# Performance work log

Hardware: AMD Instinct MI355X
Metric: run time of the kernel (lower is better)

## Reference

```python
import jax, jax.numpy as jnp
import numpy as np

ALPHA = 0.2  # LeakyReLU negative slope
NEG_INF = -9e15


def setup_inputs() -> dict:
    key = jax.random.key(0)
    k1, k2, k3, k4, k5 = jax.random.split(key, 5)
    B, N, F_in, F_out = 1, 8192, 256, 128
    h = jax.random.normal(k1, (B, N, F_in), dtype=jnp.float32)
    adj_mat = jax.random.randint(k2, (B, N, N), 0, 2, dtype=jnp.int32)
    W = jax.random.normal(k3, (F_out, F_in), dtype=jnp.float32) * 0.05
    b = jax.random.normal(k4, (F_out,), dtype=jnp.float32) * 0.05
    a = jax.random.normal(k5, (2 * F_out, 1), dtype=jnp.float32) * 0.05
    return {"h": h, "adj_mat": adj_mat, "W": W, "b": b, "a": a}


def reference(h, adj_mat, W, b, a):
    # Wh: (B, N, F_out)
    Wh = jnp.einsum('bnf,of->bno', h, W) + b
    F_out = W.shape[0]
    # Original builds concat[Wh_i, Wh_j] @ a. Equivalent: a1.Wh_i + a2.Wh_j.
    a1 = a[:F_out, 0]
    a2 = a[F_out:, 0]
    s1 = Wh @ a1  # (B, N) source-i contribution
    s2 = Wh @ a2  # (B, N) source-j contribution
    e = s1[:, :, None] + s2[:, None, :]  # (B, N, N)
    e = jnp.where(e >= 0, e, ALPHA * e)  # LeakyReLU
    e = jnp.where(adj_mat > 0, e, NEG_INF)
    attention = jax.nn.softmax(e, axis=1)  # softmax over dim=1, as in the source
    h_prime = jnp.einsum('bij,bjf->bif', attention, Wh)
    return jax.nn.elu(h_prime)
```

## Files before the change

### kernel.cpp

```cpp
#include <hip/hip_runtime.h>

#define NN 8192
#define FI 256
#define FO 128
#define GAT_ALPHA 0.2f

typedef _Float16 f16x8 __attribute__((ext_vector_type(8)));
typedef _Float16 f16x2 __attribute__((ext_vector_type(2)));
typedef float f32x4 __attribute__((ext_vector_type(4)));
typedef unsigned char uchar;
typedef unsigned int uint32;

__global__ __launch_bounds__(256) void k1_wh(const float* __restrict__ h,
                                             const float* __restrict__ W,
                                             const float* __restrict__ bias,
                                             float* __restrict__ Wh) {
  __shared__ float hs[32][FI + 1];
  __shared__ float wt[32][FO];
  const int t = threadIdx.x;
  const int j0 = blockIdx.x * 32;
  {
    const int row = t >> 3, c0 = (t & 7) * 32;
    const float* src = h + (size_t)(j0 + row) * FI + c0;
#pragma unroll
    for (int e = 0; e < 8; ++e) {
      float4 v = *(const float4*)(src + 4 * e);
      hs[row][c0 + 4 * e + 0] = v.x;
      hs[row][c0 + 4 * e + 1] = v.y;
      hs[row][c0 + 4 * e + 2] = v.z;
      hs[row][c0 + 4 * e + 3] = v.w;
    }
  }
  const int f4 = (t & 31) * 4;
  const int r0 = (t >> 5) * 4;
  float acc[4][4];
#pragma unroll
  for (int r = 0; r < 4; ++r)
#pragma unroll
    for (int e = 0; e < 4; ++e) acc[r][e] = 0.f;

  for (int kc = 0; kc < FI; kc += 32) {
    __syncthreads();
    {
      const int f = t >> 1, kb = (t & 1) * 16;
      const float* wsrc = W + (size_t)f * FI + kc + kb;
#pragma unroll
      for (int e = 0; e < 16; ++e) wt[kb + e][f] = wsrc[e];
    }
    __syncthreads();
#pragma unroll
    for (int k = 0; k < 32; ++k) {
      const float4 wv = *(const float4*)&wt[k][f4];
      float hv[4];
#pragma unroll
      for (int r = 0; r < 4; ++r) hv[r] = hs[r0 + r][kc + k];
#pragma unroll
      for (int r = 0; r < 4; ++r) {
        acc[r][0] += hv[r] * wv.x;
        acc[r][1] += hv[r] * wv.y;
        acc[r][2] += hv[r] * wv.z;
        acc[r][3] += hv[r] * wv.w;
      }
    }
  }
  const float4 bv = *(const float4*)&bias[f4];
#pragma unroll
  for (int r = 0; r < 4; ++r) {
    float4 o;
    o.x = acc[r][0] + bv.x;
    o.y = acc[r][1] + bv.y;
    o.z = acc[r][2] + bv.z;
    o.w = acc[r][3] + bv.w;
    *(float4*)&Wh[(size_t)(j0 + r0 + r) * FO + f4] = o;
  }
}

__global__ __launch_bounds__(256) void k1b_sv(const float* __restrict__ Wh,
                                              const float* __restrict__ a,
                                              float4* __restrict__ r4,
                                              float4* __restrict__ c4,
                                              float2* __restrict__ r2,
                                              _Float16* __restrict__ ey16,
                                              _Float16* __restrict__ ez16,
                                              float* __restrict__ s2x,
                                              float* __restrict__ corr) {
  if (blockIdx.x == 0 && threadIdx.x < FO) corr[threadIdx.x] = 0.f;
  const int lane = threadIdx.x & 63;
  const int j = blockIdx.x * 4 + (threadIdx.x >> 6);
  const float* row = Wh + (size_t)j * FO;
  const float w0 = row[lane], w1 = row[lane + 64];
  float s1 = w0 * a[lane] + w1 * a[lane + 64];
  float s2 = w0 * a[FO + lane] + w1 * a[FO + lane + 64];
#pragma unroll
  for (int o = 32; o >= 1; o >>= 1) {
    s1 += __shfl_xor(s1, o);
    s2 += __shfl_xor(s2, o);
  }
  if (lane == 0) {
    const float e1 = expf(s1), e1a = expf(GAT_ALPHA * s1);
    const float e2 = expf(s2), e2a = expf(GAT_ALPHA * s2);
    float4 rv; rv.x = s1; rv.y = e1; rv.z = e1a; rv.w = 0.f;
    float4 cv; cv.x = s2; cv.y = e2; cv.z = e2a; cv.w = 0.f;
    r4[j] = rv;
    c4[j] = cv;
    r2[j] = make_float2(e1, e1a);
    ey16[j] = (_Float16)e2;
    ez16[j] = (_Float16)e2a;
    s2x[j] = s2;
  }
}

__global__ __launch_bounds__(256) void k2_stats(const int* __restrict__ adj,
                                                const float4* __restrict__ r4,
                                                const float* __restrict__ s2x,
                                                uchar* __restrict__ bitsB,
                                                float2* __restrict__ zpart) {
  __shared__ float4 rs[64];
  const int t = threadIdx.x;
  const int jc = blockIdx.x & 3;
  const int ic = blockIdx.x >> 2;
  const int i0 = ic * 64;
  const int j0 = jc * 2048 + t * 8;
  if (t < 64) rs[t] = r4[i0 + t];
  const float4 ca = *(const float4*)(s2x + j0);
  const float4 cb = *(const float4*)(s2x + j0 + 4);
  const float cx[8] = {ca.x, ca.y, ca.z, ca.w, cb.x, cb.y, cb.z, cb.w};
  float accP[8], accN[8];
#pragma unroll
  for (int e = 0; e < 8; ++e) { accP[e] = 0.f; accN[e] = 0.f; }
  __syncthreads();
  const int4* ap = (const int4*)(adj + (size_t)i0 * NN + j0);
  uchar* bp = bitsB + (size_t)i0 * (NN / 8) + jc * 256 + t;
  for (int ir = 0; ir < 64; ir += 8) {
    int4 av[8][2];
#pragma unroll
    for (int u = 0; u < 8; ++u) {
      av[u][0] = ap[(size_t)(ir + u) * (NN / 4)];
      av[u][1] = ap[(size_t)(ir + u) * (NN / 4) + 1];
    }
#pragma unroll
    for (int u = 0; u < 8; ++u) {
      const float4 ri = rs[ir + u];
      const int aa[8] = {av[u][0].x, av[u][0].y, av[u][0].z, av[u][0].w,
                         av[u][1].x, av[u][1].y, av[u][1].z, av[u][1].w};
      uint32 byte = 0;
#pragma unroll
      for (int e = 0; e < 8; ++e) {
        const bool act = aa[e] > 0;
        byte |= act ? (1u << e) : 0u;
        const bool pos = (ri.x + cx[e]) >= 0.f;
        accP[e] += (act && pos) ? ri.y : 0.f;
        accN[e] += (act && !pos) ? ri.z : 0.f;
      }
      bp[(size_t)(ir + u) * (NN / 8)] = (uchar)byte;
    }
  }
  float2* zp = zpart + (size_t)ic * NN + j0;
#pragma unroll
  for (int e = 0; e < 8; ++e) zp[e] = make_float2(accP[e], accN[e]);
}

__global__ __launch_bounds__(256) void k3_scale(const float* __restrict__ Wh,
                                                const float4* __restrict__ c4,
                                                const float2* __restrict__ zpart,
                                                _Float16* __restrict__ Wfrag,
                                                float* __restrict__ corr) {
  __shared__ float rz[64];
  __shared__ int emp[64];
  __shared__ float2 psum[256];
  __shared__ __align__(16) _Float16 tile[FO * 64];
  const int t = threadIdx.x;
  const int j0 = blockIdx.x * 64;
  {
    const int jl = t & 63, q = t >> 6;
    float p = 0.f, n = 0.f;
    for (int ic = q * 32; ic < q * 32 + 32; ++ic) {
      const float2 z = zpart[(size_t)ic * NN + j0 + jl];
      p += z.x;
      n += z.y;
    }
    psum[t] = make_float2(p, n);
  }
  __syncthreads();
  if (t < 64) {
    const float p = psum[t].x + psum[64 + t].x + psum[128 + t].x + psum[192 + t].x;
    const float n = psum[t].y + psum[64 + t].y + psum[128 + t].y + psum[192 + t].y;
    const float4 cj = c4[j0 + t];
    const float Z = cj.y * p + cj.z * n;
    rz[t] = (Z > 0.f) ? 1.f / Z : 0.f;
    emp[t] = (Z > 0.f) ? 0 : 1;
  }
  __syncthreads();
  const int f = t & 127, half = t >> 7;
  const unsigned swf = (unsigned)((f & 7) << 4);
  for (int r = half; r < 64; r += 2) {
    const float v = Wh[(size_t)(j0 + r) * FO + f];
    *(_Float16*)((char*)tile + f * 128 + (((unsigned)(r * 2)) ^ swf)) =
        (_Float16)(v * rz[r]);
    if (emp[r]) atomicAdd(&corr[f], v * (1.f / 8192.f));
  }
  __syncthreads();
#pragma unroll
  for (int q = 0; q < 4; ++q) {
    const int G = t + 256 * q;
    const int kcfb = G >> 6, gl = G & 63;
    const int kc = kcfb >> 3, fb = kcfb & 7;
    const int gf = fb * 16 + (gl & 15);
    const int jloc = kc * 32 + (gl >> 4) * 8;
    const f16x8 v = *(const f16x8*)((const char*)tile + gf * 128 +
                                    (((unsigned)(jloc * 2)) ^ ((unsigned)((gf & 7) << 4))));
    ((f16x8*)Wfrag)[(size_t)(((j0 >> 5) + kc) * 8 + fb) * 64 + gl] = v;
  }
}

#define BARRIER_LDS()                                          \
  do {                                                         \
    __builtin_amdgcn_sched_barrier(0);                         \
    asm volatile("s_waitcnt lgkmcnt(0)" ::: "memory");         \
    __builtin_amdgcn_s_barrier();                              \
    __builtin_amdgcn_sched_barrier(0);                         \
  } while (0)

__global__ __launch_bounds__(512, 4) void k4_main(const uchar* __restrict__ bitsB,
                                                  const float2* __restrict__ r2,
                                                  const _Float16* __restrict__ ey16,
                                                  const _Float16* __restrict__ ez16,
                                                  const _Float16* __restrict__ Wfrag,
                                                  float* __restrict__ part) {
  __shared__ __align__(16) _Float16 P[2][64 * 64];
  __shared__ uint32 lut[256][4];
  const int t = threadIdx.x;
  const int rowtile = blockIdx.x >> 2;
  const int kq = blockIdx.x & 3;
  const int rowbase = rowtile * 64;
  const int koff = kq * 2048;

  if (t < 256) {
#pragma unroll
    for (int p = 0; p < 4; ++p) {
      const uint32 lo = ((t >> (2 * p)) & 1) ? 0x0000FFFFu : 0u;
      const uint32 hi = ((t >> (2 * p + 1)) & 1) ? 0xFFFF0000u : 0u;
      lut[t][p] = lo | hi;
    }
  }

  const int pr = t >> 3, jq = t & 7;
  const float2 rr = r2[rowbase + pr];
  const f16x2 rx2 = {(_Float16)rr.x, (_Float16)rr.x};
  const f16x2 ry2 = {(_Float16)rr.y, (_Float16)rr.y};
  const uchar* bp = bitsB + (size_t)(rowbase + pr) * (NN / 8) + (koff >> 3) + jq;
  const _Float16* eyp = ey16 + koff + jq * 8;
  const _Float16* ezp = ez16 + koff + jq * 8;
  char* const pdst0 = (char*)&P[0][0] + pr * 128 + (((unsigned)(jq * 16)) ^ ((unsigned)((pr & 7) << 4)));
  char* const pdst1 = (char*)&P[1][0] + pr * 128 + (((unsigned)(jq * 16)) ^ ((unsigned)((pr & 7) << 4)));

  const int lane = t & 63, wave = t >> 6;
  const int wr = wave >> 2, wc = wave & 3;
  const int kgrp = lane >> 4, l15 = lane & 15;
  const unsigned asw = (unsigned)((l15 & 7) << 4);
  const int ar0 = (wr * 32 + l15) * 128;
  const int ar1 = ar0 + 16 * 128;

  f32x4 acc00 = {0.f, 0.f, 0.f, 0.f}, acc01 = {0.f, 0.f, 0.f, 0.f};
  f32x4 acc10 = {0.f, 0.f, 0.f, 0.f}, acc11 = {0.f, 0.f, 0.f, 0.f};

  uchar mb0, mb1;
  uint4 ey0, ez0, ey1, ez1;
  f16x8 B000, B001, B010, B011, B100, B101, B110, B111;

#define LOADALL(S, MB, EY, EZ, Bq00, Bq01, Bq10, Bq11)                              \
  do {                                                                              \
    MB = bp[(S) * 8];                                                               \
    EY = *(const uint4*)(eyp + (S) * 64);                                           \
    EZ = *(const uint4*)(ezp + (S) * 64);                                           \
    const _Float16* _b = Wfrag + ((size_t)((kq * 64 + (S) * 2) * 8 + wc * 2) * 64 + lane) * 8; \
    Bq00 = *(const f16x8*)(_b);                                                     \
    Bq01 = *(const f16x8*)(_b + 512);                                               \
    Bq10 = *(const f16x8*)(_b + 4096);                                              \
    Bq11 = *(const f16x8*)(_b + 4096 + 512);                                        \
  } while (0)

#define PGEN(DST, MB, EY, EZ)                                                        \
  do {                                                                               \
    const uint4 _m = *(const uint4*)(&lut[MB][0]);                                   \
    const uint32 _eys[4] = {EY.x, EY.y, EY.z, EY.w};                                 \
    const uint32 _ezs[4] = {EZ.x, EZ.y, EZ.z, EZ.w};                                 \
    const uint32 _ms[4] = {_m.x, _m.y, _m.z, _m.w};                                  \
    uint32 _o[4];                                                                    \
    _Pragma("unroll") for (int _p = 0; _p < 4; ++_p) {                               \
      const f16x2 _a = __builtin_bit_cast(f16x2, _eys[_p]) * rx2;                    \
      const f16x2 _b2 = __builtin_bit_cast(f16x2, _ezs[_p]) * ry2;                   \
      const f16x2 _mx = __builtin_elementwise_max(_a, _b2);                          \
      _o[_p] = __builtin_bit_cast(uint32, _mx) & _ms[_p];                            \
    }                                                                                \
    uint4 _st; _st.x = _o[0]; _st.y = _o[1]; _st.z = _o[2]; _st.w = _o[3];           \
    *(uint4*)(DST) = _st;                                                            \
  } while (0)

#define DO_MFMA(BUF, Bq00, Bq01, Bq10, Bq11)                                        \
  do {                                                                              \
    const char* _Pb = (const char*)&P[BUF][0];                                      \
    const f16x8 a00 = *(const f16x8*)(_Pb + ar0 + ((((unsigned)(kgrp * 16))) ^ asw));        \
    const f16x8 a01 = *(const f16x8*)(_Pb + ar0 + (((unsigned)(64 + kgrp * 16)) ^ asw));     \
    const f16x8 a10 = *(const f16x8*)(_Pb + ar1 + ((((unsigned)(kgrp * 16))) ^ asw));        \
    const f16x8 a11 = *(const f16x8*)(_Pb + ar1 + (((unsigned)(64 + kgrp * 16)) ^ asw));     \
    __builtin_amdgcn_s_setprio(1);                                                  \
    acc00 = __builtin_amdgcn_mfma_f32_16x16x32_f16(a00, Bq00, acc00, 0, 0, 0);      \
    acc01 = __builtin_amdgcn_mfma_f32_16x16x32_f16(a00, Bq01, acc01, 0, 0, 0);      \
    acc10 = __builtin_amdgcn_mfma_f32_16x16x32_f16(a10, Bq00, acc10, 0, 0, 0);      \
    acc11 = __builtin_amdgcn_mfma_f32_16x16x32_f16(a10, Bq01, acc11, 0, 0, 0);      \
    acc00 = __builtin_amdgcn_mfma_f32_16x16x32_f16(a01, Bq10, acc00, 0, 0, 0);      \
    acc01 = __builtin_amdgcn_mfma_f32_16x16x32_f16(a01, Bq11, acc01, 0, 0, 0);      \
    acc10 = __builtin_amdgcn_mfma_f32_16x16x32_f16(a11, Bq10, acc10, 0, 0, 0);      \
    acc11 = __builtin_amdgcn_mfma_f32_16x16x32_f16(a11, Bq11, acc11, 0, 0, 0);      \
    __builtin_amdgcn_s_setprio(0);                                                  \
  } while (0)

  LOADALL(0, mb0, ey0, ez0, B000, B001, B010, B011);
  LOADALL(1, mb1, ey1, ez1, B100, B101, B110, B111);
  __syncthreads();
  PGEN(pdst0, mb0, ey0, ez0);
  BARRIER_LDS();

  for (int s = 0; s < 32; s += 2) {
    PGEN(pdst1, mb1, ey1, ez1);
    DO_MFMA(0, B000, B001, B010, B011);
    if (s + 2 < 32) LOADALL(s + 2, mb0, ey0, ez0, B000, B001, B010, B011);
    BARRIER_LDS();
    DO_MFMA(1, B100, B101, B110, B111);
    if (s + 2 < 32) PGEN(pdst0, mb0, ey0, ez0);
    if (s + 3 < 32) LOADALL(s + 3, mb1, ey1, ez1, B100, B101, B110, B111);
    BARRIER_LDS();
  }

#undef LOADALL
#undef PGEN
#undef DO_MFMA

  const int orow = rowbase + wr * 32 + kgrp * 4;
  const int ocol = wc * 32 + l15;
  float* aP = part + (size_t)kq * NN * FO + (size_t)orow * FO + ocol;
#pragma unroll
  for (int r = 0; r < 4; ++r) {
    aP[(size_t)r * FO] = acc00[r];
    aP[(size_t)r * FO + 16] = acc01[r];
    aP[(size_t)(16 + r) * FO] = acc10[r];
    aP[(size_t)(16 + r) * FO + 16] = acc11[r];
  }
}

__global__ __launch_bounds__(256) void k5_fin(const float* __restrict__ part,
                                              const float* __restrict__ corr,
                                              float* __restrict__ out) {
  const int idx = blockIdx.x * 256 + threadIdx.x;
  const float4 p0 = ((const float4*)part)[idx];
  const float4 p1 = ((const float4*)(part + (size_t)NN * FO))[idx];
  const float4 p2 = ((const float4*)(part + (size_t)2 * NN * FO))[idx];
  const float4 p3 = ((const float4*)(part + (size_t)3 * NN * FO))[idx];
  const float4 c = ((const float4*)corr)[idx & 31];
  float4 v;
  v.x = p0.x + p1.x + p2.x + p3.x + c.x;
  v.y = p0.y + p1.y + p2.y + p3.y + c.y;
  v.z = p0.z + p1.z + p2.z + p3.z + c.z;
  v.w = p0.w + p1.w + p2.w + p3.w + c.w;
  v.x = (v.x > 0.f) ? v.x : (expf(v.x) - 1.f);
  v.y = (v.y > 0.f) ? v.y : (expf(v.y) - 1.f);
  v.z = (v.z > 0.f) ? v.z : (expf(v.z) - 1.f);
  v.w = (v.w > 0.f) ? v.w : (expf(v.w) - 1.f);
  ((float4*)out)[idx] = v;
}

extern "C" void kernel_launch(void* const* d_in, const int* in_sizes, int n_in,
                              void* d_out, int out_size, void* d_ws, size_t ws_size,
                              hipStream_t stream) {
  const float* h = (const float*)d_in[0];
  const int* adj = (const int*)d_in[1];
  const float* W = (const float*)d_in[2];
  const float* b = (const float*)d_in[3];
  const float* a = (const float*)d_in[4];
  float* out = (float*)d_out;
  char* ws = (char*)d_ws;

  float* Wh = (float*)(ws + 0);
  _Float16* Wfrag = (_Float16*)(ws + 0x400000);
  uchar* bits = (uchar*)(ws + 0x600000);
  float2* zpart = (float2*)(ws + 0xE00000);
  float4* r4 = (float4*)(ws + 0x1600000);
  float4* c4 = (float4*)(ws + 0x1620000);
  float2* r2 = (float2*)(ws + 0x1640000);
  _Float16* ey16 = (_Float16*)(ws + 0x1650000);
  _Float16* ez16 = (_Float16*)(ws + 0x1654000);
  float* s2x = (float*)(ws + 0x1658000);
  float* corr = (float*)(ws + 0x1660000);
  float* part = (float*)(ws + 0x1700000);

  k1_wh<<<NN / 32, 256, 0, stream>>>(h, W, b, Wh);
  k1b_sv<<<NN / 4, 256, 0, stream>>>(Wh, a, r4, c4, r2, ey16, ez16, s2x, corr);
  k2_stats<<<512, 256, 0, stream>>>(adj, r4, s2x, bits, zpart);
  k3_scale<<<NN / 64, 256, 0, stream>>>(Wh, c4, zpart, Wfrag, corr);
  k4_main<<<512, 512, 0, stream>>>(bits, r2, ey16, ez16, Wfrag, part);
  k5_fin<<<(NN * FO / 4) / 256, 256, 0, stream>>>(part, corr, out);
}
```

Baseline: 125.1 us.

## Fuse score computation into Wh GEMM and halve k4 row tile size

The attention-score reduction and exponentials (formerly a separate k1b_sv launch) are now computed in the epilogue of the Wh GEMM kernel using 32-lane shuffles, removing one launch and a re-read of Wh. Separately, the main aggregation kernel switches from 64-row tiles with 512 threads to 32-row tiles with 256 threads and twice as many blocks, giving more blocks for scheduling at the cost of halving B-fragment reuse per block. The per-wave B fragment loads are now amortized over fewer rows, increasing Wfrag traffic.

```diff
diff --git a/kernel.cpp b/kernel.cpp
--- a/kernel.cpp
+++ b/kernel.cpp
@@ -14,11 +14,20 @@
 __global__ __launch_bounds__(256) void k1_wh(const float* __restrict__ h,
                                              const float* __restrict__ W,
                                              const float* __restrict__ bias,
-                                             float* __restrict__ Wh) {
+                                             const float* __restrict__ a,
+                                             float* __restrict__ Wh,
+                                             float4* __restrict__ r4,
+                                             float4* __restrict__ c4,
+                                             float2* __restrict__ r2,
+                                             _Float16* __restrict__ ey16,
+                                             _Float16* __restrict__ ez16,
+                                             float* __restrict__ s2x,
+                                             float* __restrict__ corr) {
   __shared__ float hs[32][FI + 1];
   __shared__ float wt[32][FO];
   const int t = threadIdx.x;
   const int j0 = blockIdx.x * 32;
+  if (blockIdx.x == 0 && t < FO) corr[t] = 0.f;
   {
     const int row = t >> 3, c0 = (t & 7) * 32;
     const float* src = h + (size_t)(j0 + row) * FI + c0;
@@ -64,6 +73,9 @@
     }
   }
   const float4 bv = *(const float4*)&bias[f4];
+  const float4 a1v = *(const float4*)&a[f4];
+  const float4 a2v = *(const float4*)&a[FO + f4];
+  float s1p[4], s2p[4];
 #pragma unroll
   for (int r = 0; r < 4; ++r) {
     float4 o;
@@ -72,41 +84,33 @@
     o.z = acc[r][2] + bv.z;
     o.w = acc[r][3] + bv.w;
     *(float4*)&Wh[(size_t)(j0 + r0 + r) * FO + f4] = o;
-  }
-}
-
-__global__ __launch_bounds__(256) void k1b_sv(const float* __restrict__ Wh,
-                                              const float* __restrict__ a,
-                                              float4* __restrict__ r4,
-                                              float4* __restrict__ c4,
-                                              float2* __restrict__ r2,
-                                              _Float16* __restrict__ ey16,
-                                              _Float16* __restrict__ ez16,
-                                              float* __restrict__ s2x,
-                                              float* __restrict__ corr) {
-  if (blockIdx.x == 0 && threadIdx.x < FO) corr[threadIdx.x] = 0.f;
-  const int lane = threadIdx.x & 63;
-  const int j = blockIdx.x * 4 + (threadIdx.x >> 6);
-  const float* row = Wh + (size_t)j * FO;
-  const float w0 = row[lane], w1 = row[lane + 64];
-  float s1 = w0 * a[lane] + w1 * a[lane + 64];
-  float s2 = w0 * a[FO + lane] + w1 * a[FO + lane + 64];
-#pragma unroll
-  for (int o = 32; o >= 1; o >>= 1) {
-    s1 += __shfl_xor(s1, o);
-    s2 += __shfl_xor(s2, o);
-  }
-  if (lane == 0) {
-    const float e1 = expf(s1), e1a = expf(GAT_ALPHA * s1);
-    const float e2 = expf(s2), e2a = expf(GAT_ALPHA * s2);
-    float4 rv; rv.x = s1; rv.y = e1; rv.z = e1a; rv.w = 0.f;
-    float4 cv; cv.x = s2; cv.y = e2; cv.z = e2a; cv.w = 0.f;
-    r4[j] = rv;
-    c4[j] = cv;
-    r2[j] = make_float2(e1, e1a);
-    ey16[j] = (_Float16)e2;
-    ez16[j] = (_Float16)e2a;
-    s2x[j] = s2;
+    s1p[r] = o.x * a1v.x + o.y * a1v.y + o.z * a1v.z + o.w * a1v.w;
+    s2p[r] = o.x * a2v.x + o.y * a2v.y + o.z * a2v.z + o.w * a2v.w;
+  }
+#pragma unroll
+  for (int m = 16; m >= 1; m >>= 1) {
+#pragma unroll
+    for (int r = 0; r < 4; ++r) {
+      s1p[r] += __shfl_xor(s1p[r], m);
+      s2p[r] += __shfl_xor(s2p[r], m);
+    }
+  }
+  if ((t & 31) == 0) {
+#pragma unroll
+    for (int r = 0; r < 4; ++r) {
+      const int j = j0 + r0 + r;
+      const float s1 = s1p[r], s2 = s2p[r];
+      const float e1 = expf(s1), e1a = expf(GAT_ALPHA * s1);
+      const float e2 = expf(s2), e2a = expf(GAT_ALPHA * s2);
+      float4 rv; rv.x = s1; rv.y = e1; rv.z = e1a; rv.w = 0.f;
+      float4 cv; cv.x = s2; cv.y = e2; cv.z = e2a; cv.w = 0.f;
+      r4[j] = rv;
+      c4[j] = cv;
+      r2[j] = make_float2(e1, e1a);
+      ey16[j] = (_Float16)e2;
+      ez16[j] = (_Float16)e2a;
+      s2x[j] = s2;
+    }
   }
 }
 
@@ -221,21 +225,21 @@
     __builtin_amdgcn_sched_barrier(0);                         \
   } while (0)
 
-__global__ __launch_bounds__(512, 4) void k4_main(const uchar* __restrict__ bitsB,
-                                                  const float2* __restrict__ r2,
-                                                  const _Float16* __restrict__ ey16,
-                                                  const _Float16* __restrict__ ez16,
-                                                  const _Float16* __restrict__ Wfrag,
-                                                  float* __restrict__ part) {
-  __shared__ __align__(16) _Float16 P[2][64 * 64];
+__global__ __launch_bounds__(256) void k4_main(const uchar* __restrict__ bitsB,
+                                               const float2* __restrict__ r2,
+                                               const _Float16* __restrict__ ey16,
+                                               const _Float16* __restrict__ ez16,
+                                               const _Float16* __restrict__ Wfrag,
+                                               float* __restrict__ part) {
+  __shared__ __align__(16) _Float16 P[2][32 * 64];
   __shared__ uint32 lut[256][4];
   const int t = threadIdx.x;
   const int rowtile = blockIdx.x >> 2;
   const int kq = blockIdx.x & 3;
-  const int rowbase = rowtile * 64;
+  const int rowbase = rowtile * 32;
   const int koff = kq * 2048;
 
-  if (t < 256) {
+  {
 #pragma unroll
     for (int p = 0; p < 4; ++p) {
       const uint32 lo = ((t >> (2 * p)) & 1) ? 0x0000FFFFu : 0u;
@@ -254,11 +258,10 @@
   char* const pdst0 = (char*)&P[0][0] + pr * 128 + (((unsigned)(jq * 16)) ^ ((unsigned)((pr & 7) << 4)));
   char* const pdst1 = (char*)&P[1][0] + pr * 128 + (((unsigned)(jq * 16)) ^ ((unsigned)((pr & 7) << 4)));
 
-  const int lane = t & 63, wave = t >> 6;
-  const int wr = wave >> 2, wc = wave & 3;
+  const int lane = t & 63, wc = t >> 6;
   const int kgrp = lane >> 4, l15 = lane & 15;
   const unsigned asw = (unsigned)((l15 & 7) << 4);
-  const int ar0 = (wr * 32 + l15) * 128;
+  const int ar0 = l15 * 128;
   const int ar1 = ar0 + 16 * 128;
 
   f32x4 acc00 = {0.f, 0.f, 0.f, 0.f}, acc01 = {0.f, 0.f, 0.f, 0.f};
@@ -337,7 +340,7 @@
 #undef PGEN
 #undef DO_MFMA
 
-  const int orow = rowbase + wr * 32 + kgrp * 4;
+  const int orow = rowbase + kgrp * 4;
   const int ocol = wc * 32 + l15;
   float* aP = part + (size_t)kq * NN * FO + (size_t)orow * FO + ocol;
 #pragma unroll
@@ -394,10 +397,9 @@
   float* corr = (float*)(ws + 0x1660000);
   float* part = (float*)(ws + 0x1700000);
 
-  k1_wh<<<NN / 32, 256, 0, stream>>>(h, W, b, Wh);
-  k1b_sv<<<NN / 4, 256, 0, stream>>>(Wh, a, r4, c4, r2, ey16, ez16, s2x, corr);
+  k1_wh<<<NN / 32, 256, 0, stream>>>(h, W, b, a, Wh, r4, c4, r2, ey16, ez16, s2x, corr);
   k2_stats<<<512, 256, 0, stream>>>(adj, r4, s2x, bits, zpart);
   k3_scale<<<NN / 64, 256, 0, stream>>>(Wh, c4, zpart, Wfrag, corr);
-  k4_main<<<512, 512, 0, stream>>>(bits, r2, ey16, ez16, Wfrag, part);
+  k4_main<<<1024, 256, 0, stream>>>(bits, r2, ey16, ez16, Wfrag, part);
   k5_fin<<<(NN * FO / 4) / 256, 256, 0, stream>>>(part, corr, out);
 }
```

Measured after the change: 124.9 us. No clear change (-0.2%).
